# Kernel optimization log

Hardware: AMD Instinct MI355X
Metric: run time of the kernel (lower is better)

Reference implementation:

```python
import jax, jax.numpy as jnp
import numpy as np

N_NODES = 50000
D = 512
N_EDGES = 1600000

def setup_inputs() -> dict:
    key = jax.random.key(0)
    ks = jax.random.split(key, 5)
    x = jax.random.normal(ks[0], (N_NODES, D), dtype=jnp.float32)
    W = jax.random.normal(ks[1], (D, D), dtype=jnp.float32) * (1.0 / np.sqrt(D))
    b = jnp.zeros((D,), dtype=jnp.float32)
    edge_weight = jax.random.uniform(ks[2], (N_EDGES,), dtype=jnp.float32)
    edge_src = jax.random.randint(ks[3], (N_EDGES,), 0, N_NODES, dtype=jnp.int32)
    edge_dst = jax.random.randint(ks[4], (N_EDGES,), 0, N_NODES, dtype=jnp.int32)
    return {"x": x, "W": W, "b": b, "edge_weight": edge_weight,
            "edge_src": edge_src, "edge_dst": edge_dst}

def reference(x, W, b, edge_weight, edge_src, edge_dst):
    # GraphConvolution: support = x @ W; out = spmm(adj, support) + b
    support = x @ W                                  # [N, D] dense GEMM
    msgs = support[edge_src] * edge_weight[:, None]  # gather + scale [E, D]
    agg = jax.ops.segment_sum(msgs, edge_dst, num_segments=x.shape[0])  # [N, D]
    gc_out = agg + b
    # GCN2: relu then residual
    return jax.nn.relu(gc_out) + x
```

## Files before the change

kernel.cpp:

```cpp
#include <hip/hip_runtime.h>

#define N_NODES 50000
#define DIM 512
#define KCAT 1024
#define N_EDGES 1600000
#define CHSHIFT 12
#define NCHUNK 13
#define CAPC 20
#define PBLK 4096
#define DPW 12
#define TAIL (N_NODES - PBLK * DPW)

typedef __attribute__((ext_vector_type(8))) short short8;
typedef __attribute__((ext_vector_type(8))) unsigned short ushort8;
typedef __attribute__((ext_vector_type(4))) float floatx4;

__device__ __forceinline__ unsigned short f2bf(float v) {
    unsigned u = __float_as_uint(v);
    unsigned r = u + 0x7FFF + ((u >> 16) & 1);
    return (unsigned short)(r >> 16);
}
__device__ __forceinline__ float bf2f(unsigned short h) {
    return __uint_as_float((unsigned)h << 16);
}
__device__ __forceinline__ void stage16(const char* g, char* l) {
    __builtin_amdgcn_global_load_lds((const __attribute__((address_space(1))) void*)g,
                                     (__attribute__((address_space(3))) void*)l, 16, 0, 0);
}

__global__ __launch_bounds__(256) void convert_x(const float* __restrict__ x,
                                                 unsigned short* __restrict__ xcat) {
    const int t = blockIdx.x * 256 + threadIdx.x;
    if (t >= N_NODES * 64) return;
    const int row = t >> 6;
    const int kc = t & 63;
    const int blk = kc >> 3;
    const int c = kc & 7;
    const int cSw = c ^ (row & 7);

    const floatx4 v0 = __builtin_nontemporal_load((const floatx4*)&x[row * DIM + kc * 8]);
    const floatx4 v1 = __builtin_nontemporal_load((const floatx4*)&x[row * DIM + kc * 8 + 4]);
    float v[8] = {v0.x, v0.y, v0.z, v0.w, v1.x, v1.y, v1.z, v1.w};
    unsigned short h[8], l[8];
#pragma unroll
    for (int j = 0; j < 8; j++) {
        h[j] = f2bf(v[j]);
        l[j] = f2bf(v[j] - bf2f(h[j]));
    }
    const int o = row * KCAT + blk * 64 + cSw * 8;
    *(short8*)&xcat[o] = *(short8*)h;
    *(short8*)&xcat[o + DIM] = *(short8*)l;
}

__global__ __launch_bounds__(256) void convert_w(const float* __restrict__ W,
                                                 unsigned short* __restrict__ wcat) {
    const int t = blockIdx.x * 256 + threadIdx.x;
    if (t >= DIM * 64) return;
    const int n = t >> 6;
    const int kc = t & 63;
    const int blk = kc >> 3;
    const int c = kc & 7;
    const int cSw = c ^ (n & 7);

    unsigned short h[8];
#pragma unroll
    for (int j = 0; j < 8; j++) h[j] = f2bf(W[(kc * 8 + j) * DIM + n]);
    const int o = n * KCAT + blk * 64 + cSw * 8;
    *(short8*)&wcat[o] = *(short8*)h;
    *(short8*)&wcat[o + DIM] = *(short8*)h;
}

__global__ __launch_bounds__(256, 3) void gemm_cat(const unsigned short* __restrict__ A,
                                                   const unsigned short* __restrict__ B,
                                                   unsigned short* __restrict__ Cb, int M) {
    __shared__ __align__(128) char smem[32768];

    const int tid = threadIdx.x;
    const int row0 = blockIdx.y * 128;
    const int col0 = blockIdx.x * 128;

    int srow[4], schk[4];
#pragma unroll
    for (int i = 0; i < 4; i++) {
        const int q = i * 256 + tid;
        srow[i] = q >> 3;
        schk[i] = q & 7;
    }

    const int l = tid & 63;
    const int w = tid >> 6;
    const int wm = w & 1, wn = w >> 1;
    const int lrow = l & 15;
    const int kg = l >> 4;
    const int s = l & 7;

    int offA[4][2], offB[4][2];
#pragma unroll
    for (int mt = 0; mt < 4; mt++)
#pragma unroll
        for (int h = 0; h < 2; h++) {
            const int chunk = (kg + 4 * h) ^ s;
            offA[mt][h] = (wm * 64 + mt * 16 + lrow) * 128 + chunk * 16;
            offB[mt][h] = 16384 + (wn * 64 + mt * 16 + lrow) * 128 + chunk * 16;
        }

    floatx4 acc[4][4];
#pragma unroll
    for (int i = 0; i < 4; i++)
#pragma unroll
        for (int j = 0; j < 4; j++) acc[i][j] = (floatx4)(0.f);

    const char* A8 = (const char*)A;
    const char* B8 = (const char*)B;

    for (int kblk = 0; kblk < 16; kblk++) {
        __syncthreads();
#pragma unroll
        for (int i = 0; i < 4; i++) {
            const int q16 = (i * 256 + tid) * 16;
            const size_t ga = (size_t)min(row0 + srow[i], M - 1) * (KCAT * 2)
                              + kblk * 128 + schk[i] * 16;
            const size_t gb = (size_t)(col0 + srow[i]) * (KCAT * 2)
                              + kblk * 128 + schk[i] * 16;
            stage16(A8 + ga, smem + q16);
            stage16(B8 + gb, smem + 16384 + q16);
        }
        __syncthreads();

#pragma unroll
        for (int h = 0; h < 2; h++) {
            short8 bf[4];
#pragma unroll
            for (int nt = 0; nt < 4; nt++) bf[nt] = *(const short8*)(smem + offB[nt][h]);
#pragma unroll
            for (int mt = 0; mt < 4; mt++) {
                const short8 af = *(const short8*)(smem + offA[mt][h]);
#pragma unroll
                for (int nt = 0; nt < 4; nt++)
                    acc[mt][nt] = __builtin_amdgcn_mfma_f32_16x16x32_bf16(
                        af, bf[nt], acc[mt][nt], 0, 0, 0);
            }
        }
    }

    const int crow0 = row0 + wm * 64;
    const int ccol0 = col0 + wn * 64;
#pragma unroll
    for (int mt = 0; mt < 4; mt++) {
        const int rbase = crow0 + mt * 16 + kg * 4;
#pragma unroll
        for (int nt = 0; nt < 4; nt++) {
            const int cc = ccol0 + nt * 16 + lrow;
#pragma unroll
            for (int r = 0; r < 4; r++) {
                const int gr = rbase + r;
                if (gr < M) Cb[(size_t)gr * DIM + cc] = f2bf(acc[mt][nt][r]);
            }
        }
    }
}

__global__ __launch_bounds__(256) void gcn_build_edges(const int* __restrict__ esrc,
                                                       const int* __restrict__ edst,
                                                       const float* __restrict__ ew,
                                                       int* __restrict__ cursor,
                                                       unsigned int* __restrict__ table) {
    const int e = blockIdx.x * 256 + threadIdx.x;
    if (e >= N_EDGES) return;
    const int d = __builtin_nontemporal_load(&edst[e]);
    const int s = __builtin_nontemporal_load(&esrc[e]);
    const float w = __builtin_nontemporal_load(&ew[e]);
    const int ch = s >> CHSHIFT;
    const int pos = atomicAdd(&cursor[ch * N_NODES + d], 1);
    if (pos < CAPC) {
        const unsigned rec = (unsigned)s | ((unsigned)f2bf(w) << 16);
        __builtin_nontemporal_store(
            rec, &table[((size_t)ch * N_NODES + d) * CAPC + pos]);
    }
}

__device__ __forceinline__ void write_node(int n, int tid, const float* acc,
                                           const float* bb,
                                           const unsigned short* __restrict__ xcat,
                                           float* __restrict__ out) {
    const int c8 = tid * 8;
    const int xoff = n * KCAT + (tid >> 3) * 64 + (((tid & 7) ^ (n & 7)) * 8);
    const ushort8 xb = __builtin_nontemporal_load((const ushort8*)&xcat[xoff]);
    float o[8];
#pragma unroll
    for (int j = 0; j < 8; j++) o[j] = fmaxf(acc[j] + bb[j], 0.f) + bf2f(xb[j]);
    floatx4 o0, o1;
    o0.x = o[0]; o0.y = o[1]; o0.z = o[2]; o0.w = o[3];
    o1.x = o[4]; o1.y = o[5]; o1.z = o[6]; o1.w = o[7];
    __builtin_nontemporal_store(o0, (floatx4*)&out[(size_t)n * DIM + c8]);
    __builtin_nontemporal_store(o1, (floatx4*)&out[(size_t)n * DIM + c8 + 4]);
}

__global__ __launch_bounds__(64, 4) void gcn_aggregate_pers(
        const unsigned short* __restrict__ sup,
        const int* __restrict__ cursor,
        const unsigned int* __restrict__ table,
        const unsigned short* __restrict__ xcat,
        const float* __restrict__ b,
        float* __restrict__ out) {
    const int w = blockIdx.x;
    const int tid = threadIdx.x;
    const int c8 = tid * 8;

    float acc[DPW][8];
#pragma unroll
    for (int k = 0; k < DPW; k++)
#pragma unroll
        for (int j = 0; j < 8; j++) acc[k][j] = 0.f;

    const unsigned short* supc = sup + c8;

    for (int c = 0; c < NCHUNK; c++) {
#pragma unroll
        for (int k = 0; k < DPW; k++) {
            const int dst = w + k * PBLK;
            const int cnt = min(cursor[c * N_NODES + dst], CAPC);
            const size_t segbase = ((size_t)c * N_NODES + dst) * CAPC;
#pragma unroll 2
            for (int i = 0; i < cnt; i++) {
                const unsigned rec = table[segbase + i];
                const float wt = bf2f((unsigned short)(rec >> 16));
                const ushort8 v = *(const ushort8*)(supc + (size_t)(rec & 0xFFFFu) * DIM);
#pragma unroll
                for (int j = 0; j < 8; j++) acc[k][j] = fmaf(wt, bf2f(v[j]), acc[k][j]);
            }
        }
        asm volatile("" ::: "memory");
    }

    const float4 b0 = *(const float4*)&b[c8];
    const float4 b1 = *(const float4*)&b[c8 + 4];
    const float bb[8] = {b0.x, b0.y, b0.z, b0.w, b1.x, b1.y, b1.z, b1.w};
#pragma unroll
    for (int k = 0; k < DPW; k++)
        write_node(w + k * PBLK, tid, acc[k], bb, xcat, out);
}

__global__ __launch_bounds__(64) void gcn_aggregate_tail(
        const unsigned short* __restrict__ sup,
        const int* __restrict__ cursor,
        const unsigned int* __restrict__ table,
        const unsigned short* __restrict__ xcat,
        const float* __restrict__ b,
        float* __restrict__ out) {
    const int n = PBLK * DPW + blockIdx.x;
    const int tid = threadIdx.x;
    const int c8 = tid * 8;

    float acc[8];
#pragma unroll
    for (int j = 0; j < 8; j++) acc[j] = 0.f;

    const unsigned short* supc = sup + c8;

    for (int c = 0; c < NCHUNK; c++) {
        const int cnt = min(cursor[c * N_NODES + n], CAPC);
        const size_t segbase = ((size_t)c * N_NODES + n) * CAPC;
#pragma unroll 2
        for (int i = 0; i < cnt; i++) {
            const unsigned rec = table[segbase + i];
            const float wt = bf2f((unsigned short)(rec >> 16));
            const ushort8 v = *(const ushort8*)(supc + (size_t)(rec & 0xFFFFu) * DIM);
#pragma unroll
            for (int j = 0; j < 8; j++) acc[j] = fmaf(wt, bf2f(v[j]), acc[j]);
        }
    }

    const float4 b0 = *(const float4*)&b[c8];
    const float4 b1 = *(const float4*)&b[c8 + 4];
    const float bb[8] = {b0.x, b0.y, b0.z, b0.w, b1.x, b1.y, b1.z, b1.w};
    write_node(n, tid, acc, bb, xcat, out);
}

extern "C" void kernel_launch(void* const* d_in, const int* in_sizes, int n_in,
                              void* d_out, int out_size, void* d_ws, size_t ws_size,
                              hipStream_t stream) {
    const float* x = (const float*)d_in[0];
    const float* W = (const float*)d_in[1];
    const float* b = (const float*)d_in[2];
    const float* ew = (const float*)d_in[3];
    const int* esrc = (const int*)d_in[4];
    const int* edst = (const int*)d_in[5];
    float* out = (float*)d_out;

    char* ws = (char*)d_ws;
    size_t off = 0;
    unsigned short* support = (unsigned short*)(ws + off); off += (size_t)N_NODES * DIM * 2;
    int* cursor = (int*)(ws + off);                   off += (size_t)NCHUNK * N_NODES * 4;
    unsigned int* table = (unsigned int*)(ws + off);  off += (size_t)NCHUNK * N_NODES * CAPC * 4;
    unsigned short* xcat = (unsigned short*)(ws + off); off += (size_t)N_NODES * KCAT * 2;
    unsigned short* wcat = (unsigned short*)(ws + off); off += (size_t)DIM * KCAT * 2;

    (void)hipMemsetAsync(cursor, 0, (size_t)NCHUNK * N_NODES * sizeof(int), stream);

    convert_w<<<(DIM * 64 + 255) / 256, 256, 0, stream>>>(W, wcat);
    convert_x<<<(N_NODES * 64 + 255) / 256, 256, 0, stream>>>(x, xcat);

    gcn_build_edges<<<(N_EDGES + 255) / 256, 256, 0, stream>>>(esrc, edst, ew,
                                                               cursor, table);

    dim3 gemm_grid(DIM / 128, (N_NODES + 127) / 128);
    gemm_cat<<<gemm_grid, 256, 0, stream>>>(xcat, wcat, support, N_NODES);

    gcn_aggregate_pers<<<PBLK, 64, 0, stream>>>(support, cursor, table, xcat, b, out);
    gcn_aggregate_tail<<<TAIL, 64, 0, stream>>>(support, cursor, table, xcat, b, out);
}
```

Before: 655.4 us.

## Switch GEMM to single fp16 pass, pack per-wave counts, contiguous node blocks

Replaces the split-bf16 (hi+lo, K=1024) GEMM with a single fp16 GEMM over K=512, halving MFMA work and the staged A/B bytes, and stores support and the residual copy of x in fp16. A new kernel packs per-chunk edge counts for each block of 12 consecutive nodes into 16 bytes, so the aggregation reads one vector per chunk instead of 12 scattered cursor values. Aggregation now gives each block 12 contiguous destination nodes and drops the separate tail kernel. fp16 range and precision could differ from the bf16 hi/lo scheme, and the residual x now carries fp16 rounding.

Result: slower. 675.6 us (+3.1%).

```diff
diff --git a/kernel.cpp b/kernel.cpp
--- a/kernel.cpp
+++ b/kernel.cpp
@@ -2,18 +2,17 @@
 
 #define N_NODES 50000
 #define DIM 512
-#define KCAT 1024
 #define N_EDGES 1600000
 #define CHSHIFT 12
 #define NCHUNK 13
 #define CAPC 20
-#define PBLK 4096
 #define DPW 12
-#define TAIL (N_NODES - PBLK * DPW)
+#define NWAVE 4167
 
 typedef __attribute__((ext_vector_type(8))) short short8;
 typedef __attribute__((ext_vector_type(8))) unsigned short ushort8;
 typedef __attribute__((ext_vector_type(4))) float floatx4;
+typedef __attribute__((ext_vector_type(8))) _Float16 half8;
 
 __device__ __forceinline__ unsigned short f2bf(float v) {
     unsigned u = __float_as_uint(v);
@@ -29,7 +28,7 @@
 }
 
 __global__ __launch_bounds__(256) void convert_x(const float* __restrict__ x,
-                                                 unsigned short* __restrict__ xcat) {
+                                                 _Float16* __restrict__ xh) {
     const int t = blockIdx.x * 256 + threadIdx.x;
     if (t >= N_NODES * 64) return;
     const int row = t >> 6;
@@ -40,20 +39,15 @@
 
     const floatx4 v0 = __builtin_nontemporal_load((const floatx4*)&x[row * DIM + kc * 8]);
     const floatx4 v1 = __builtin_nontemporal_load((const floatx4*)&x[row * DIM + kc * 8 + 4]);
-    float v[8] = {v0.x, v0.y, v0.z, v0.w, v1.x, v1.y, v1.z, v1.w};
-    unsigned short h[8], l[8];
-#pragma unroll
-    for (int j = 0; j < 8; j++) {
-        h[j] = f2bf(v[j]);
-        l[j] = f2bf(v[j] - bf2f(h[j]));
-    }
-    const int o = row * KCAT + blk * 64 + cSw * 8;
-    *(short8*)&xcat[o] = *(short8*)h;
-    *(short8*)&xcat[o + DIM] = *(short8*)l;
+    const float v[8] = {v0.x, v0.y, v0.z, v0.w, v1.x, v1.y, v1.z, v1.w};
+    half8 h;
+#pragma unroll
+    for (int j = 0; j < 8; j++) h[j] = (_Float16)v[j];
+    *(half8*)&xh[row * DIM + blk * 64 + cSw * 8] = h;
 }
 
 __global__ __launch_bounds__(256) void convert_w(const float* __restrict__ W,
-                                                 unsigned short* __restrict__ wcat) {
+                                                 _Float16* __restrict__ wh) {
     const int t = blockIdx.x * 256 + threadIdx.x;
     if (t >= DIM * 64) return;
     const int n = t >> 6;
@@ -62,17 +56,15 @@
     const int c = kc & 7;
     const int cSw = c ^ (n & 7);
 
-    unsigned short h[8];
-#pragma unroll
-    for (int j = 0; j < 8; j++) h[j] = f2bf(W[(kc * 8 + j) * DIM + n]);
-    const int o = n * KCAT + blk * 64 + cSw * 8;
-    *(short8*)&wcat[o] = *(short8*)h;
-    *(short8*)&wcat[o + DIM] = *(short8*)h;
-}
-
-__global__ __launch_bounds__(256, 3) void gemm_cat(const unsigned short* __restrict__ A,
-                                                   const unsigned short* __restrict__ B,
-                                                   unsigned short* __restrict__ Cb, int M) {
+    half8 h;
+#pragma unroll
+    for (int j = 0; j < 8; j++) h[j] = (_Float16)W[(kc * 8 + j) * DIM + n];
+    *(half8*)&wh[n * DIM + blk * 64 + cSw * 8] = h;
+}
+
+__global__ __launch_bounds__(256, 3) void gemm_f16(const _Float16* __restrict__ A,
+                                                   const _Float16* __restrict__ B,
+                                                   _Float16* __restrict__ Cb, int M) {
     __shared__ __align__(128) char smem[32768];
 
     const int tid = threadIdx.x;
@@ -113,14 +105,14 @@
     const char* A8 = (const char*)A;
     const char* B8 = (const char*)B;
 
-    for (int kblk = 0; kblk < 16; kblk++) {
+    for (int kblk = 0; kblk < 8; kblk++) {
         __syncthreads();
 #pragma unroll
         for (int i = 0; i < 4; i++) {
             const int q16 = (i * 256 + tid) * 16;
-            const size_t ga = (size_t)min(row0 + srow[i], M - 1) * (KCAT * 2)
+            const size_t ga = (size_t)min(row0 + srow[i], M - 1) * (DIM * 2)
                               + kblk * 128 + schk[i] * 16;
-            const size_t gb = (size_t)(col0 + srow[i]) * (KCAT * 2)
+            const size_t gb = (size_t)(col0 + srow[i]) * (DIM * 2)
                               + kblk * 128 + schk[i] * 16;
             stage16(A8 + ga, smem + q16);
             stage16(B8 + gb, smem + 16384 + q16);
@@ -129,15 +121,15 @@
 
 #pragma unroll
         for (int h = 0; h < 2; h++) {
-            short8 bf[4];
-#pragma unroll
-            for (int nt = 0; nt < 4; nt++) bf[nt] = *(const short8*)(smem + offB[nt][h]);
+            half8 bf[4];
+#pragma unroll
+            for (int nt = 0; nt < 4; nt++) bf[nt] = *(const half8*)(smem + offB[nt][h]);
 #pragma unroll
             for (int mt = 0; mt < 4; mt++) {
-                const short8 af = *(const short8*)(smem + offA[mt][h]);
+                const half8 af = *(const half8*)(smem + offA[mt][h]);
 #pragma unroll
                 for (int nt = 0; nt < 4; nt++)
-                    acc[mt][nt] = __builtin_amdgcn_mfma_f32_16x16x32_bf16(
+                    acc[mt][nt] = __builtin_amdgcn_mfma_f32_16x16x32_f16(
                         af, bf[nt], acc[mt][nt], 0, 0, 0);
             }
         }
@@ -154,7 +146,7 @@
 #pragma unroll
             for (int r = 0; r < 4; r++) {
                 const int gr = rbase + r;
-                if (gr < M) Cb[(size_t)gr * DIM + cc] = f2bf(acc[mt][nt][r]);
+                if (gr < M) Cb[(size_t)gr * DIM + cc] = (_Float16)acc[mt][nt][r];
             }
         }
     }
@@ -179,31 +171,31 @@
     }
 }
 
-__device__ __forceinline__ void write_node(int n, int tid, const float* acc,
-                                           const float* bb,
-                                           const unsigned short* __restrict__ xcat,
-                                           float* __restrict__ out) {
-    const int c8 = tid * 8;
-    const int xoff = n * KCAT + (tid >> 3) * 64 + (((tid & 7) ^ (n & 7)) * 8);
-    const ushort8 xb = __builtin_nontemporal_load((const ushort8*)&xcat[xoff]);
-    float o[8];
-#pragma unroll
-    for (int j = 0; j < 8; j++) o[j] = fmaxf(acc[j] + bb[j], 0.f) + bf2f(xb[j]);
-    floatx4 o0, o1;
-    o0.x = o[0]; o0.y = o[1]; o0.z = o[2]; o0.w = o[3];
-    o1.x = o[4]; o1.y = o[5]; o1.z = o[6]; o1.w = o[7];
-    __builtin_nontemporal_store(o0, (floatx4*)&out[(size_t)n * DIM + c8]);
-    __builtin_nontemporal_store(o1, (floatx4*)&out[(size_t)n * DIM + c8 + 4]);
+__global__ __launch_bounds__(256) void gcn_pack_counts(const int* __restrict__ cursor,
+                                                       unsigned char* __restrict__ pcntT) {
+    const int c = blockIdx.y;
+    const int w = blockIdx.x * 256 + threadIdx.x;
+    if (w >= NWAVE) return;
+    unsigned wd[4] = {0, 0, 0, 0};
+#pragma unroll
+    for (int k = 0; k < DPW; k++) {
+        const int dst = w * DPW + k;
+        const unsigned cnt = (dst < N_NODES)
+            ? (unsigned)min(cursor[c * N_NODES + dst], CAPC) : 0u;
+        wd[k >> 2] |= cnt << ((k & 3) * 8);
+    }
+    uint4 o; o.x = wd[0]; o.y = wd[1]; o.z = wd[2]; o.w = wd[3];
+    *(uint4*)(pcntT + ((size_t)c * NWAVE + w) * 16) = o;
 }
 
 __global__ __launch_bounds__(64, 4) void gcn_aggregate_pers(
-        const unsigned short* __restrict__ sup,
-        const int* __restrict__ cursor,
+        const _Float16* __restrict__ sup,
+        const unsigned char* __restrict__ pcntT,
         const unsigned int* __restrict__ table,
-        const unsigned short* __restrict__ xcat,
+        const _Float16* __restrict__ xh,
         const float* __restrict__ b,
         float* __restrict__ out) {
-    const int w = blockIdx.x;
+    const int blk = blockIdx.x;
     const int tid = threadIdx.x;
     const int c8 = tid * 8;
 
@@ -213,21 +205,24 @@
 #pragma unroll
         for (int j = 0; j < 8; j++) acc[k][j] = 0.f;
 
-    const unsigned short* supc = sup + c8;
+    const _Float16* supc = sup + c8;
 
     for (int c = 0; c < NCHUNK; c++) {
+        const uint4 pcv = *(const uint4*)(pcntT + ((size_t)c * NWAVE + blk) * 16);
+        const unsigned pw[4] = {pcv.x, pcv.y, pcv.z, pcv.w};
 #pragma unroll
         for (int k = 0; k < DPW; k++) {
-            const int dst = w + k * PBLK;
-            const int cnt = min(cursor[c * N_NODES + dst], CAPC);
+            const int dst = blk * DPW + k;
+            const int cnt = (int)((pw[k >> 2] >> ((k & 3) * 8)) & 0xFFu);
             const size_t segbase = ((size_t)c * N_NODES + dst) * CAPC;
 #pragma unroll 2
             for (int i = 0; i < cnt; i++) {
                 const unsigned rec = table[segbase + i];
                 const float wt = bf2f((unsigned short)(rec >> 16));
-                const ushort8 v = *(const ushort8*)(supc + (size_t)(rec & 0xFFFFu) * DIM);
-#pragma unroll
-                for (int j = 0; j < 8; j++) acc[k][j] = fmaf(wt, bf2f(v[j]), acc[k][j]);
+                const half8 v = *(const half8*)(supc + (size_t)(rec & 0xFFFFu) * DIM);
+#pragma unroll
+                for (int j = 0; j < 8; j++)
+                    acc[k][j] = fmaf(wt, (float)v[j], acc[k][j]);
             }
         }
         asm volatile("" ::: "memory");
@@ -237,44 +232,21 @@
     const float4 b1 = *(const float4*)&b[c8 + 4];
     const float bb[8] = {b0.x, b0.y, b0.z, b0.w, b1.x, b1.y, b1.z, b1.w};
 #pragma unroll
-    for (int k = 0; k < DPW; k++)
-        write_node(w + k * PBLK, tid, acc[k], bb, xcat, out);
-}
-
-__global__ __launch_bounds__(64) void gcn_aggregate_tail(
-        const unsigned short* __restrict__ sup,
-        const int* __restrict__ cursor,
-        const unsigned int* __restrict__ table,
-        const unsigned short* __restrict__ xcat,
-        const float* __restrict__ b,
-        float* __restrict__ out) {
-    const int n = PBLK * DPW + blockIdx.x;
-    const int tid = threadIdx.x;
-    const int c8 = tid * 8;
-
-    float acc[8];
-#pragma unroll
-    for (int j = 0; j < 8; j++) acc[j] = 0.f;
-
-    const unsigned short* supc = sup + c8;
-
-    for (int c = 0; c < NCHUNK; c++) {
-        const int cnt = min(cursor[c * N_NODES + n], CAPC);
-        const size_t segbase = ((size_t)c * N_NODES + n) * CAPC;
-#pragma unroll 2
-        for (int i = 0; i < cnt; i++) {
-            const unsigned rec = table[segbase + i];
-            const float wt = bf2f((unsigned short)(rec >> 16));
-            const ushort8 v = *(const ushort8*)(supc + (size_t)(rec & 0xFFFFu) * DIM);
-#pragma unroll
-            for (int j = 0; j < 8; j++) acc[j] = fmaf(wt, bf2f(v[j]), acc[j]);
-        }
-    }
-
-    const float4 b0 = *(const float4*)&b[c8];
-    const float4 b1 = *(const float4*)&b[c8 + 4];
-    const float bb[8] = {b0.x, b0.y, b0.z, b0.w, b1.x, b1.y, b1.z, b1.w};
-    write_node(n, tid, acc, bb, xcat, out);
+    for (int k = 0; k < DPW; k++) {
+        const int n = blk * DPW + k;
+        if (n >= N_NODES) continue;
+        const int xoff = n * DIM + (tid >> 3) * 64 + (((tid & 7) ^ (n & 7)) * 8);
+        const half8 xb = *(const half8*)&xh[xoff];
+        float o[8];
+#pragma unroll
+        for (int j = 0; j < 8; j++)
+            o[j] = fmaxf(acc[k][j] + bb[j], 0.f) + (float)xb[j];
+        floatx4 o0, o1;
+        o0.x = o[0]; o0.y = o[1]; o0.z = o[2]; o0.w = o[3];
+        o1.x = o[4]; o1.y = o[5]; o1.z = o[6]; o1.w = o[7];
+        __builtin_nontemporal_store(o0, (floatx4*)&out[(size_t)n * DIM + c8]);
+        __builtin_nontemporal_store(o1, (floatx4*)&out[(size_t)n * DIM + c8 + 4]);
+    }
 }
 
 extern "C" void kernel_launch(void* const* d_in, const int* in_sizes, int n_in,
@@ -290,23 +262,25 @@
 
     char* ws = (char*)d_ws;
     size_t off = 0;
-    unsigned short* support = (unsigned short*)(ws + off); off += (size_t)N_NODES * DIM * 2;
-    int* cursor = (int*)(ws + off);                   off += (size_t)NCHUNK * N_NODES * 4;
-    unsigned int* table = (unsigned int*)(ws + off);  off += (size_t)NCHUNK * N_NODES * CAPC * 4;
-    unsigned short* xcat = (unsigned short*)(ws + off); off += (size_t)N_NODES * KCAT * 2;
-    unsigned short* wcat = (unsigned short*)(ws + off); off += (size_t)DIM * KCAT * 2;
+    _Float16* support = (_Float16*)(ws + off);       off += (size_t)N_NODES * DIM * 2;
+    int* cursor = (int*)(ws + off);                  off += (size_t)NCHUNK * N_NODES * 4;
+    unsigned int* table = (unsigned int*)(ws + off); off += (size_t)NCHUNK * N_NODES * CAPC * 4;
+    unsigned char* pcntT = (unsigned char*)(ws + off); off += (size_t)NCHUNK * NWAVE * 16;
+    _Float16* xh = (_Float16*)(ws + off);            off += (size_t)N_NODES * DIM * 2;
+    _Float16* wh = (_Float16*)(ws + off);            off += (size_t)DIM * DIM * 2;
 
     (void)hipMemsetAsync(cursor, 0, (size_t)NCHUNK * N_NODES * sizeof(int), stream);
 
-    convert_w<<<(DIM * 64 + 255) / 256, 256, 0, stream>>>(W, wcat);
-    convert_x<<<(N_NODES * 64 + 255) / 256, 256, 0, stream>>>(x, xcat);
+    convert_w<<<(DIM * 64 + 255) / 256, 256, 0, stream>>>(W, wh);
+    convert_x<<<(N_NODES * 64 + 255) / 256, 256, 0, stream>>>(x, xh);
 
     gcn_build_edges<<<(N_EDGES + 255) / 256, 256, 0, stream>>>(esrc, edst, ew,
                                                                cursor, table);
+    dim3 pack_grid((NWAVE + 255) / 256, NCHUNK);
+    gcn_pack_counts<<<pack_grid, 256, 0, stream>>>(cursor, pcntT);
 
     dim3 gemm_grid(DIM / 128, (N_NODES + 127) / 128);
-    gemm_cat<<<gemm_grid, 256, 0, stream>>>(xcat, wcat, support, N_NODES);
-
-    gcn_aggregate_pers<<<PBLK, 64, 0, stream>>>(support, cursor, table, xcat, b, out);
-    gcn_aggregate_tail<<<TAIL, 64, 0, stream>>>(support, cursor, table, xcat, b, out);
-}
+    gemm_f16<<<gemm_grid, 256, 0, stream>>>(xh, wh, support, N_NODES);
+
+    gcn_aggregate_pers<<<NWAVE, 64, 0, stream>>>(support, pcntT, table, xh, b, out);
+}
```
